# Performance work log

Hardware: AMD Instinct MI355X
Metric: run time of the kernel (lower is better)

Reference implementation:

```python
import jax, jax.numpy as jnp
import numpy as np

IMG = 1024.0          # image height == width
OUT = 7               # roi_size
RATIO = 2             # sampling_ratio
SCALE = 1.0 / 32.0    # spatial_scale
BBOX_W = (10.0, 10.0, 5.0, 5.0)
DWH_CLIP = float(np.log(1000.0 / 16.0))


def _bilinear(feat, ys, xs):
    """feat [C,H,W]; ys [N,P,1], xs [N,1,P] -> [C,N,P,P] (torchvision semantics)."""
    C, H, W = feat.shape
    valid = (ys > -1.0) & (ys < H) & (xs > -1.0) & (xs < W)
    y = jnp.clip(ys, 0.0, H - 1.0)
    x = jnp.clip(xs, 0.0, W - 1.0)
    y0 = jnp.floor(y).astype(jnp.int32)
    x0 = jnp.floor(x).astype(jnp.int32)
    y1 = jnp.minimum(y0 + 1, H - 1)
    x1 = jnp.minimum(x0 + 1, W - 1)
    ly = y - y0
    lx = x - x0
    hy = 1.0 - ly
    hx = 1.0 - lx
    v = (feat[:, y0, x0] * (hy * hx) + feat[:, y0, x1] * (hy * lx)
         + feat[:, y1, x0] * (ly * hx) + feat[:, y1, x1] * (ly * lx))
    return jnp.where(valid, v, 0.0)


def _roi_align_image(feat, rois):
    """feat [C,H,W], rois [N,4] xyxy in image coords -> [N,C,OUT,OUT]."""
    b = rois * SCALE
    x1, y1 = b[:, 0], b[:, 1]
    rw = jnp.maximum(b[:, 2] - x1, 1.0)
    rh = jnp.maximum(b[:, 3] - y1, 1.0)
    bw = rw / OUT
    bh = rh / OUT
    # sub-bin sample offsets: [OUT*RATIO] positions along each roi edge
    g = (jnp.arange(OUT, dtype=jnp.float32)[:, None]
         + (jnp.arange(RATIO, dtype=jnp.float32)[None, :] + 0.5) / RATIO).reshape(-1)
    ys = y1[:, None] + g[None, :] * bh[:, None]   # [N, OUT*RATIO]
    xs = x1[:, None] + g[None, :] * bw[:, None]
    v = _bilinear(feat, ys[:, :, None], xs[:, None, :])          # [C,N,P,P]
    C = feat.shape[0]
    v = v.reshape(C, -1, OUT, RATIO, OUT, RATIO).mean(axis=(3, 5))  # avg over samples
    return jnp.transpose(v, (1, 0, 2, 3))


def _decode(deltas, proposals):
    """deltas [R,K*4], proposals [R,4] -> clipped boxes [R,K,4]."""
    wx, wy, ww, wh = BBOX_W
    pw = proposals[:, 2] - proposals[:, 0]
    ph = proposals[:, 3] - proposals[:, 1]
    cx = proposals[:, 0] + 0.5 * pw
    cy = proposals[:, 1] + 0.5 * ph
    d = deltas.reshape(deltas.shape[0], -1, 4)
    dx = d[..., 0] / wx
    dy = d[..., 1] / wy
    dw = jnp.minimum(d[..., 2] / ww, DWH_CLIP)
    dh = jnp.minimum(d[..., 3] / wh, DWH_CLIP)
    pcx = dx * pw[:, None] + cx[:, None]
    pcy = dy * ph[:, None] + cy[:, None]
    ppw = jnp.exp(dw) * pw[:, None]
    pph = jnp.exp(dh) * ph[:, None]
    boxes = jnp.stack([pcx - 0.5 * ppw, pcy - 0.5 * pph,
                       pcx + 0.5 * ppw, pcy + 0.5 * pph], axis=-1)
    return jnp.clip(boxes, 0.0, IMG)  # clip_boxes_to_image


def setup_inputs() -> dict:
    key = jax.random.key(0)
    ks = jax.random.split(key, 8)
    B, N, C, H, W = 2, 1024, 256, 32, 32
    feat_dim = C * OUT * OUT  # 12544
    features = jax.random.normal(ks[0], (B, C, H, W), dtype=jnp.float32)
    cxy = jax.random.uniform(ks[1], (B, N, 2), minval=0.0, maxval=IMG)
    wh = jax.random.uniform(ks[2], (B, N, 2), minval=16.0, maxval=256.0)
    p1 = jnp.clip(cxy - 0.5 * wh, 0.0, IMG)
    p2 = jnp.clip(cxy + 0.5 * wh, 0.0, IMG)
    proposals = jnp.concatenate([p1, p2], axis=-1)  # [B,N,4] valid xyxy
    w1 = jax.random.normal(ks[3], (1024, feat_dim), dtype=jnp.float32) * 0.01
    w2 = jax.random.normal(ks[4], (1024, 1024), dtype=jnp.float32) * 0.01
    wc = jax.random.normal(ks[5], (2, 1024), dtype=jnp.float32) * 0.01
    wb = jax.random.normal(ks[6], (8, 1024), dtype=jnp.float32) * 0.001
    return {"features": features, "proposals": proposals,
            "w1": w1, "b1": jnp.zeros((1024,), jnp.float32),
            "w2": w2, "b2": jnp.zeros((1024,), jnp.float32),
            "wc": wc, "bc": jnp.zeros((2,), jnp.float32),
            "wb": wb, "bb": jnp.zeros((8,), jnp.float32)}


def reference(features, proposals, w1, b1, w2, b2, wc, bc, wb, bb):
    pooled = jax.vmap(_roi_align_image)(features, proposals)   # [B,N,C,7,7]
    B, N = pooled.shape[:2]
    x = pooled.reshape(B * N, -1)                               # flatten(start_dim=1)
    x = jax.nn.relu(x @ w1.T + b1)
    x = jax.nn.relu(x @ w2.T + b2)
    cls_scores = x @ wc.T + bc                                  # [R, num_classes]
    bbox_deltas = x @ wb.T + bb                                 # [R, num_classes*4]
    pred_boxes = _decode(bbox_deltas, proposals.reshape(-1, 4)) # [R, num_classes, 4]
    pred_scores = jax.nn.softmax(cls_scores, axis=-1)
    return cls_scores, bbox_deltas, pred_boxes, pred_scores
```

## Files before the change

kernel.cpp:

```cpp
#include <hip/hip_runtime.h>
#include <hip/hip_bf16.h>
#include <stdint.h>

typedef __attribute__((ext_vector_type(8))) short bf16x8;
typedef __attribute__((ext_vector_type(4))) float f32x4;

__device__ __forceinline__ ushort f2bf(float f) {
    union { float f; uint32_t u; } c; c.f = f;
    uint32_t u = c.u;
    uint32_t r = (u + 0x7FFFu + ((u >> 16) & 1u)) >> 16;
    return (ushort)r;
}

__device__ __forceinline__ void load16_to_lds(const void* gsrc, void* ldst) {
    __builtin_amdgcn_global_load_lds(
        (const __attribute__((address_space(1))) uint32_t*)gsrc,
        (__attribute__((address_space(3))) uint32_t*)ldst,
        16, 0, 0);
}

#define FENCE() asm volatile("" ::: "memory")
#define BARRIER() do { FENCE(); __builtin_amdgcn_s_barrier(); FENCE(); } while (0)
#define VMCNT(n) asm volatile("s_waitcnt vmcnt(" #n ")" ::: "memory")

__global__ __launch_bounds__(256) void f32_to_bf16_kernel(
    const float* __restrict__ in, ushort* __restrict__ out, int n)
{
    int i = (blockIdx.x * 256 + threadIdx.x) * 4;
    if (i >= n) return;
    float4 v = *(const float4*)(in + i);
    ushort4 o;
    o.x = f2bf(v.x); o.y = f2bf(v.y); o.z = f2bf(v.z); o.w = f2bf(v.w);
    *(ushort4*)(out + i) = o;
}

__global__ __launch_bounds__(256) void transpose_feat_kernel(
    const float* __restrict__ feat, float* __restrict__ featT)
{
    int bc = blockIdx.x;
    int b = bc >> 8;
    int c = bc & 255;
    const float* src = feat + (size_t)bc * 1024;
    float* dst = featT + (size_t)b * 262144 + c;
    #pragma unroll
    for (int i = 0; i < 4; ++i) {
        int p = i * 256 + threadIdx.x;
        dst[(size_t)p * 256] = src[p];
    }
}

__global__ __launch_bounds__(512) void roi_align_kernel(
    const float* __restrict__ featT, const float* __restrict__ props,
    ushort* __restrict__ pooled)
{
    int roi = blockIdx.x;
    int b = roi >> 10;
    __shared__ int   si0[28];
    __shared__ int   si1[28];
    __shared__ float sl[28];
    __shared__ float sv[28];
    __shared__ float Aw[7][10];
    __shared__ float Bw[7][10];
    __shared__ __align__(16) ushort outbuf[12544];
    int tid = threadIdx.x;
    if (tid < 28) {
        int axis = (tid >= 14) ? 1 : 0;
        int pp = tid - axis * 14;
        float c0 = props[roi * 4 + (axis ? 0 : 1)] * (1.f / 32.f);
        float c1 = props[roi * 4 + (axis ? 2 : 3)] * (1.f / 32.f);
        float sz = fmaxf(c1 - c0, 1.f);
        float bsz = sz * (1.f / 7.f);
        float g = (float)(pp >> 1) + ((float)(pp & 1) + 0.5f) * 0.5f;
        float c = c0 + g * bsz;
        float valid = (c > -1.f && c < 32.f) ? 1.f : 0.f;
        float cc = fminf(fmaxf(c, 0.f), 31.f);
        float fl = floorf(cc);
        int i0 = (int)fl;
        si0[tid] = i0;
        si1[tid] = min(i0 + 1, 31);
        sl[tid] = cc - fl;
        sv[tid] = valid;
    }
    __syncthreads();

    const int r0 = si0[0];
    const int c0 = si0[14];

    if (tid < 140) {
        int axis = tid / 70;
        int e = tid - axis * 70;
        int oy = e / 10, yy = e - oy * 10;
        int base = axis * 14;
        int org = axis ? c0 : r0;
        float wsum = 0.f;
        #pragma unroll
        for (int s = 0; s < 2; ++s) {
            int p = base + oy * 2 + s;
            float w = 0.f;
            if (si0[p] - org == yy) w += 1.f - sl[p];
            if (si1[p] - org == yy) w += sl[p];
            wsum += sv[p] * w;
        }
        wsum *= 0.5f;
        if (axis == 0) Aw[oy][yy] = wsum;
        else           Bw[oy][yy] = wsum;
    }
    __syncthreads();

    const int grp = tid >> 8;
    const int ch = tid & 255;
    const float* fbase = featT + (size_t)b * 262144 + ch;

    int xoff[10];
    #pragma unroll
    for (int x = 0; x < 10; ++x) xoff[x] = min(c0 + x, 31) * 256;

    if (grp == 0) {
        float t[4][10];
        #pragma unroll
        for (int oy = 0; oy < 4; ++oy)
            #pragma unroll
            for (int x = 0; x < 10; ++x) t[oy][x] = 0.f;
        #pragma unroll
        for (int y = 0; y < 10; ++y) {
            const float* frow = fbase + (size_t)min(r0 + y, 31) * 8192;
            float a0 = Aw[0][y], a1 = Aw[1][y], a2 = Aw[2][y], a3 = Aw[3][y];
            #pragma unroll
            for (int x = 0; x < 10; ++x) {
                float fv = frow[xoff[x]];
                t[0][x] += a0 * fv;
                t[1][x] += a1 * fv;
                t[2][x] += a2 * fv;
                t[3][x] += a3 * fv;
            }
        }
        #pragma unroll
        for (int oy = 0; oy < 4; ++oy)
            #pragma unroll
            for (int ox = 0; ox < 7; ++ox) {
                float o = 0.f;
                #pragma unroll
                for (int x = 0; x < 10; ++x) o += Bw[ox][x] * t[oy][x];
                outbuf[ch * 49 + oy * 7 + ox] = f2bf(o);
            }
    } else {
        float t[3][10];
        #pragma unroll
        for (int oy = 0; oy < 3; ++oy)
            #pragma unroll
            for (int x = 0; x < 10; ++x) t[oy][x] = 0.f;
        #pragma unroll
        for (int y = 0; y < 10; ++y) {
            const float* frow = fbase + (size_t)min(r0 + y, 31) * 8192;
            float a4 = Aw[4][y], a5 = Aw[5][y], a6 = Aw[6][y];
            #pragma unroll
            for (int x = 0; x < 10; ++x) {
                float fv = frow[xoff[x]];
                t[0][x] += a4 * fv;
                t[1][x] += a5 * fv;
                t[2][x] += a6 * fv;
            }
        }
        #pragma unroll
        for (int oy = 0; oy < 3; ++oy)
            #pragma unroll
            for (int ox = 0; ox < 7; ++ox) {
                float o = 0.f;
                #pragma unroll
                for (int x = 0; x < 10; ++x) o += Bw[ox][x] * t[oy][x];
                outbuf[ch * 49 + (4 + oy) * 7 + ox] = f2bf(o);
            }
    }
    __syncthreads();

    const uint4* src = (const uint4*)outbuf;
    uint4* dst = (uint4*)(pooled + (size_t)roi * 12544);
    #pragma unroll
    for (int i = 0; i < 4; ++i) {
        int idx = i * 512 + tid;
        if (idx < 1568) dst[idx] = src[idx];
    }
}

#define STAGE_A8(BB, HALF, KOFF) do { \
    _Pragma("unroll") for (int r_ = 0; r_ < 2; ++r_) { \
        int rbase_ = (HALF) * 128 + r_ * 64 + w * 8; \
        int row_ = rbase_ + (l >> 3); \
        int c16s_ = (l & 7) ^ (row_ & 7); \
        load16_to_lds((const char*)(Ap + (size_t)(m0 + row_) * K + (KOFF)) + c16s_ * 16, \
                      &sA[BB][rbase_][0]); \
    } } while (0)
#define STAGE_B8(BB, Q, KOFF) do { \
    _Pragma("unroll") for (int r_ = 0; r_ < 2; ++r_) { \
        int rl_ = r_ * 64 + w * 8 + (l >> 3); \
        int brow_ = ((rl_ >> 5) << 6) + (Q) * 32 + (rl_ & 31); \
        int c16s_ = (l & 7) ^ (rl_ & 7); \
        load16_to_lds((const char*)(Bp + (size_t)(n0 + brow_) * K + (KOFF)) + c16s_ * 16, \
                      &sB[BB][(Q) * 128 + r_ * 64 + w * 8][0]); \
    } } while (0)
#define PHASE8(QM, QN, STAGE_CODE, WAIT_CODE) do { \
    STAGE_CODE; \
    WAIT_CODE; \
    BARRIER(); \
    bf16x8 av_[8], bv_[4]; \
    _Pragma("unroll") for (int mm_ = 0; mm_ < 4; ++mm_) \
        _Pragma("unroll") for (int kk_ = 0; kk_ < 2; ++kk_) { \
            int lr_ = wm * 128 + (QM) * 64 + mm_ * 16 + lrow; \
            int c16s_ = (kk_ * 4 + khi) ^ (lrow & 7); \
            av_[mm_ * 2 + kk_] = *(const bf16x8*)&sA[cur][lr_][c16s_ * 8]; \
        } \
    _Pragma("unroll") for (int nn_ = 0; nn_ < 2; ++nn_) \
        _Pragma("unroll") for (int kk_ = 0; kk_ < 2; ++kk_) { \
            int lrB_ = (QN) * 128 + wn * 32 + nn_ * 16 + lrow; \
            int c16s_ = (kk_ * 4 + khi) ^ (lrow & 7); \
            bv_[nn_ * 2 + kk_] = *(const bf16x8*)&sB[cur][lrB_][c16s_ * 8]; \
        } \
    __builtin_amdgcn_s_setprio(1); \
    _Pragma("unroll") for (int mm_ = 0; mm_ < 4; ++mm_) \
        _Pragma("unroll") for (int nn_ = 0; nn_ < 2; ++nn_) \
            _Pragma("unroll") for (int kk_ = 0; kk_ < 2; ++kk_) \
                acc[(QM) * 4 + mm_][(QN) * 2 + nn_] = __builtin_amdgcn_mfma_f32_16x16x32_bf16( \
                    av_[mm_ * 2 + kk_], bv_[nn_ * 2 + kk_], acc[(QM) * 4 + mm_][(QN) * 2 + nn_], 0, 0, 0); \
    __builtin_amdgcn_s_setprio(0); \
    BARRIER(); \
} while (0)

__global__ __launch_bounds__(512) void gemm_8ph(
    const ushort* __restrict__ Ap, const ushort* __restrict__ Bp,
    float* __restrict__ part, int M, int N, int K, int klen)
{
    __shared__ __align__(16) ushort sA[2][256][64];
    __shared__ __align__(16) ushort sB[2][256][64];
    const int tid = threadIdx.x;

    const int nbx = gridDim.x, nby = gridDim.y;
    const int nwg = nbx * nby * gridDim.z;
    const int d = blockIdx.x + nbx * (blockIdx.y + nby * blockIdx.z);
    const int t = (d & 7) * (nwg >> 3) + (d >> 3);
    const int n_blk = t % nbx;
    const int m_blk = (t / nbx) % nby;
    const int k_blk = t / (nbx * nby);

    const int m0 = m_blk * 256;
    const int n0 = n_blk * 256;
    const int k_start = k_blk * klen;
    const int nt = klen >> 6;

    const int w = tid >> 6, l = tid & 63;
    const int wm = w >> 2, wn = w & 3;
    const int lrow = l & 15, khi = l >> 4;

    f32x4 acc[8][4] = {};

    {
        int k0 = k_start, k1 = k_start + 64;
        STAGE_B8(0, 0, k0);
        STAGE_A8(0, 1, k0);
        STAGE_A8(0, 0, k0);
        STAGE_B8(0, 1, k0);
        STAGE_B8(1, 0, k1);
        STAGE_A8(1, 1, k1);
    }

    int cur = 0;
    for (int T = 0; T < nt - 1; ++T) {
        const int koff1 = k_start + (T + 1) * 64;
        const int koff2 = k_start + (T + 2) * 64;
        const int nxt = cur ^ 1;
        const bool has2 = (T + 2) < nt;
        PHASE8(0, 0, { STAGE_A8(nxt, 0, koff1); }, VMCNT(8));
        PHASE8(1, 0, { STAGE_B8(nxt, 1, koff1); }, );
        PHASE8(1, 1, { if (has2) STAGE_B8(cur, 0, koff2); }, VMCNT(8));
        PHASE8(0, 1, { if (has2) STAGE_A8(cur, 1, koff2); }, );
        cur ^= 1;
    }
    PHASE8(0, 0, , VMCNT(2));
    PHASE8(1, 0, , );
    PHASE8(1, 1, , VMCNT(0));
    PHASE8(0, 1, , );

    const int r4 = (l >> 4) * 4;
    const int cc = l & 15;
    float* pb = part + (size_t)k_blk * M * N;
    #pragma unroll
    for (int m = 0; m < 8; ++m) {
        #pragma unroll
        for (int n = 0; n < 4; ++n) {
            int col = n0 + wn * 64 + n * 16 + cc;
            #pragma unroll
            for (int j = 0; j < 4; ++j) {
                int row = m0 + wm * 128 + m * 16 + r4 + j;
                pb[(size_t)row * N + col] = acc[m][n][j];
            }
        }
    }
}

__global__ __launch_bounds__(256) void gemm_bt_split(
    const ushort* __restrict__ A, const ushort* __restrict__ Bm,
    float* __restrict__ part, int M, int N, int K, int klen)
{
    constexpr int BK = 32;
    __shared__ __align__(16) ushort lA[2][128][BK];
    __shared__ __align__(16) ushort lB[2][128][BK];
    const int tid = threadIdx.x;

    const int nbx = gridDim.x, nby = gridDim.y;
    const int nwg = nbx * nby * gridDim.z;
    const int d = blockIdx.x + nbx * (blockIdx.y + nby * blockIdx.z);
    const int t = (d & 7) * (nwg >> 3) + (d >> 3);
    const int n_blk = t % nbx;
    const int m_blk = (t / nbx) % nby;
    const int k_blk = t / (nbx * nby);

    const int m0 = m_blk * 128;
    const int n0 = n_blk * 128;
    const int k_start = k_blk * klen;

    const int w = tid >> 6, l = tid & 63;
    const int wr = w >> 1, wcid = w & 1;
    const int lrow = l & 15;
    const int lkb = (((l >> 4) ^ ((lrow >> 1) & 3)) * 16);

    const int sc0 = tid, sc1 = 256 + tid;
    const int srow0 = sc0 >> 2, srow1 = sc1 >> 2;
    const int scol0 = ((sc0 & 3) ^ ((srow0 >> 1) & 3)) * 16;
    const int scol1 = ((sc1 & 3) ^ ((srow1 >> 1) & 3)) * 16;

    const int nsteps = klen / BK;

    {
        int k0 = k_start;
        load16_to_lds((const char*)(A + (size_t)(m0 + srow0) * K + k0) + scol0, ((char*)lA[0]) + sc0 * 16);
        load16_to_lds((const char*)(A + (size_t)(m0 + srow1) * K + k0) + scol1, ((char*)lA[0]) + sc1 * 16);
        load16_to_lds((const char*)(Bm + (size_t)(n0 + srow0) * K + k0) + scol0, ((char*)lB[0]) + sc0 * 16);
        load16_to_lds((const char*)(Bm + (size_t)(n0 + srow1) * K + k0) + scol1, ((char*)lB[0]) + sc1 * 16);
    }
    __syncthreads();

    f32x4 acc[4][4] = {};
    int cur = 0;

    for (int ts = 0; ts < nsteps; ++ts) {
        if (ts + 1 < nsteps) {
            int k0 = k_start + (ts + 1) * BK;
            int nxt = cur ^ 1;
            load16_to_lds((const char*)(A + (size_t)(m0 + srow0) * K + k0) + scol0, ((char*)lA[nxt]) + sc0 * 16);
            load16_to_lds((const char*)(A + (size_t)(m0 + srow1) * K + k0) + scol1, ((char*)lA[nxt]) + sc1 * 16);
            load16_to_lds((const char*)(Bm + (size_t)(n0 + srow0) * K + k0) + scol0, ((char*)lB[nxt]) + sc0 * 16);
            load16_to_lds((const char*)(Bm + (size_t)(n0 + srow1) * K + k0) + scol1, ((char*)lB[nxt]) + sc1 * 16);
        }

        bf16x8 af[4], bfr[4];
        #pragma unroll
        for (int m = 0; m < 4; ++m)
            af[m] = *(const bf16x8*)(((const char*)lA[cur]) + (wr * 64 + m * 16 + lrow) * 64 + lkb);
        #pragma unroll
        for (int n = 0; n < 4; ++n)
            bfr[n] = *(const bf16x8*)(((const char*)lB[cur]) + (wcid * 64 + n * 16 + lrow) * 64 + lkb);
        #pragma unroll
        for (int m = 0; m < 4; ++m)
            #pragma unroll
            for (int n = 0; n < 4; ++n)
                acc[m][n] = __builtin_amdgcn_mfma_f32_16x16x32_bf16(af[m], bfr[n], acc[m][n], 0, 0, 0);

        __syncthreads();
        cur ^= 1;
    }

    const int r4 = (l >> 4) * 4;
    const int cc = l & 15;
    float* pb = part + (size_t)k_blk * M * N;
    #pragma unroll
    for (int m = 0; m < 4; ++m) {
        #pragma unroll
        for (int n = 0; n < 4; ++n) {
            int col = n0 + wcid * 64 + n * 16 + cc;
            #pragma unroll
            for (int j = 0; j < 4; ++j) {
                int row = m0 + wr * 64 + m * 16 + r4 + j;
                pb[(size_t)row * N + col] = acc[m][n][j];
            }
        }
    }
}

template<bool OUT_BF16>
__global__ __launch_bounds__(256) void reduce_split_kernel(
    const float* __restrict__ part, const float* __restrict__ bias,
    void* __restrict__ out, int MN, int N, int S, int relu)
{
    int i4 = (blockIdx.x * 256 + threadIdx.x) * 4;
    if (i4 >= MN) return;
    float4 a = *(const float4*)(part + i4);
    for (int s = 1; s < S; ++s) {
        float4 b = *(const float4*)(part + (size_t)s * MN + i4);
        a.x += b.x; a.y += b.y; a.z += b.z; a.w += b.w;
    }
    int bc = i4 & (N - 1);
    float4 bv = *(const float4*)(bias + bc);
    a.x += bv.x; a.y += bv.y; a.z += bv.z; a.w += bv.w;
    if (relu) {
        a.x = fmaxf(a.x, 0.f); a.y = fmaxf(a.y, 0.f);
        a.z = fmaxf(a.z, 0.f); a.w = fmaxf(a.w, 0.f);
    }
    if (OUT_BF16) {
        ushort4 o; o.x = f2bf(a.x); o.y = f2bf(a.y); o.z = f2bf(a.z); o.w = f2bf(a.w);
        *(ushort4*)((ushort*)out + i4) = o;
    } else {
        *(float4*)((float*)out + i4) = a;
    }
}

template<bool OUT_BF16>
__global__ __launch_bounds__(256) void gemm_bt(
    const ushort* __restrict__ A, const ushort* __restrict__ Bm,
    const float* __restrict__ bias, void* __restrict__ Cout,
    int M, int N, int K, int relu)
{
    constexpr int BM = 128, BN = 64, BK = 32;
    __shared__ __align__(16) ushort lA[BM][BK];
    __shared__ __align__(16) ushort lB[BN][BK];
    const int tid = threadIdx.x;
    const int m0 = blockIdx.y * BM;
    const int n0 = blockIdx.x * BN;
    const int w = tid >> 6, l = tid & 63;
    const int wr = w >> 1, wcid = w & 1;
    const int lrow = l & 15, lk = (l >> 4) * 8;

    f32x4 acc[4][2] = {};

    for (int k0 = 0; k0 < K; k0 += BK) {
        __syncthreads();
        #pragma unroll
        for (int i = 0; i < 2; ++i) {
            int chunk = i * 256 + tid;
            int row = chunk >> 2;
            int colb = (chunk & 3) * 16;
            load16_to_lds((const char*)(A + (size_t)(m0 + row) * K + k0) + colb, ((char*)lA) + chunk * 16);
        }
        {
            int chunk = tid;
            int row = chunk >> 2;
            int colb = (chunk & 3) * 16;
            load16_to_lds((const char*)(Bm + (size_t)(n0 + row) * K + k0) + colb, ((char*)lB) + chunk * 16);
        }
        __syncthreads();

        bf16x8 af[4], bfr[2];
        #pragma unroll
        for (int m = 0; m < 4; ++m)
            af[m] = *(const bf16x8*)&lA[wr * 64 + m * 16 + lrow][lk];
        #pragma unroll
        for (int n = 0; n < 2; ++n)
            bfr[n] = *(const bf16x8*)&lB[wcid * 32 + n * 16 + lrow][lk];
        #pragma unroll
        for (int m = 0; m < 4; ++m)
            #pragma unroll
            for (int n = 0; n < 2; ++n)
                acc[m][n] = __builtin_amdgcn_mfma_f32_16x16x32_bf16(af[m], bfr[n], acc[m][n], 0, 0, 0);
    }

    const int r4 = (l >> 4) * 4;
    const int cc = l & 15;
    #pragma unroll
    for (int m = 0; m < 4; ++m) {
        #pragma unroll
        for (int n = 0; n < 2; ++n) {
            int col = n0 + wcid * 32 + n * 16 + cc;
            float bv = bias[col];
            #pragma unroll
            for (int j = 0; j < 4; ++j) {
                int row = m0 + wr * 64 + m * 16 + r4 + j;
                float v = acc[m][n][j] + bv;
                if (relu) v = fmaxf(v, 0.f);
                if (OUT_BF16) ((ushort*)Cout)[(size_t)row * N + col] = f2bf(v);
                else          ((float*)Cout)[(size_t)row * N + col] = v;
            }
        }
    }
}

__global__ __launch_bounds__(256) void heads_kernel(
    const float* __restrict__ x2,
    const float* __restrict__ wc, const float* __restrict__ bc,
    const float* __restrict__ wb, const float* __restrict__ bb,
    float* __restrict__ out)
{
    int w = threadIdx.x >> 6, l = threadIdx.x & 63;
    int row = blockIdx.x * 4 + w;
    const float* xr = x2 + (size_t)row * 1024;
    float acc[10];
    #pragma unroll
    for (int o = 0; o < 10; ++o) acc[o] = 0.f;
    for (int i = 0; i < 16; ++i) {
        int k = i * 64 + l;
        float xv = xr[k];
        #pragma unroll
        for (int o = 0; o < 2; ++o) acc[o] += xv * wc[o * 1024 + k];
        #pragma unroll
        for (int o = 0; o < 8; ++o) acc[2 + o] += xv * wb[o * 1024 + k];
    }
    #pragma unroll
    for (int o = 0; o < 10; ++o) {
        float v = acc[o];
        #pragma unroll
        for (int s = 32; s > 0; s >>= 1) v += __shfl_xor(v, s, 64);
        acc[o] = v;
    }
    if (l == 0) {
        float* cls = out;
        float* bbx = out + 2048 * 2;
        cls[row * 2 + 0] = acc[0] + bc[0];
        cls[row * 2 + 1] = acc[1] + bc[1];
        #pragma unroll
        for (int o = 0; o < 8; ++o) bbx[row * 8 + o] = acc[2 + o] + bb[o];
    }
}

__global__ __launch_bounds__(256) void decode_kernel(
    const float* __restrict__ props, float* __restrict__ out)
{
    int r = blockIdx.x * 256 + threadIdx.x;
    if (r >= 2048) return;
    const float* cls = out;
    const float* bbx = out + 4096;
    float* boxes  = out + 20480;
    float* scores = out + 36864;
    float px1 = props[r * 4 + 0], py1 = props[r * 4 + 1];
    float px2 = props[r * 4 + 2], py2 = props[r * 4 + 3];
    float pw = px2 - px1, ph = py2 - py1;
    float cx = px1 + 0.5f * pw, cy = py1 + 0.5f * ph;
    const float CLIP = 4.135166556742356f;
    #pragma unroll
    for (int k = 0; k < 2; ++k) {
        float dx = bbx[r * 8 + k * 4 + 0] * 0.1f;
        float dy = bbx[r * 8 + k * 4 + 1] * 0.1f;
        float dw = fminf(bbx[r * 8 + k * 4 + 2] * 0.2f, CLIP);
        float dh = fminf(bbx[r * 8 + k * 4 + 3] * 0.2f, CLIP);
        float pcx = dx * pw + cx, pcy = dy * ph + cy;
        float ppw = expf(dw) * pw, pph = expf(dh) * ph;
        float v0 = pcx - 0.5f * ppw, v1 = pcy - 0.5f * pph;
        float v2 = pcx + 0.5f * ppw, v3 = pcy + 0.5f * pph;
        boxes[r * 8 + k * 4 + 0] = fminf(fmaxf(v0, 0.f), 1024.f);
        boxes[r * 8 + k * 4 + 1] = fminf(fmaxf(v1, 0.f), 1024.f);
        boxes[r * 8 + k * 4 + 2] = fminf(fmaxf(v2, 0.f), 1024.f);
        boxes[r * 8 + k * 4 + 3] = fminf(fmaxf(v3, 0.f), 1024.f);
    }
    float s0 = cls[r * 2], s1 = cls[r * 2 + 1];
    float m = fmaxf(s0, s1);
    float e0 = expf(s0 - m), e1 = expf(s1 - m);
    float inv = 1.f / (e0 + e1);
    scores[r * 2 + 0] = e0 * inv;
    scores[r * 2 + 1] = e1 * inv;
}

extern "C" void kernel_launch(void* const* d_in, const int* in_sizes, int n_in,
                              void* d_out, int out_size, void* d_ws, size_t ws_size,
                              hipStream_t stream) {
    const float* feat  = (const float*)d_in[0];
    const float* props = (const float*)d_in[1];
    const float* w1    = (const float*)d_in[2];
    const float* b1    = (const float*)d_in[3];
    const float* w2    = (const float*)d_in[4];
    const float* b2    = (const float*)d_in[5];
    const float* wc    = (const float*)d_in[6];
    const float* bc    = (const float*)d_in[7];
    const float* wb    = (const float*)d_in[8];
    const float* bb    = (const float*)d_in[9];
    float* out = (float*)d_out;

    char* ws = (char*)d_ws;
    ushort* pooled = (ushort*)(ws);
    ushort* w1b    = (ushort*)(ws + 51380224);
    ushort* w2b    = (ushort*)(ws + 51380224 + 25690112);
    ushort* x1     = (ushort*)(ws + 79167488);
    float*  x2     = (float*) (ws + 83361792);
    float*  featT  = (float*) (ws + 83361792);
    float*  part   = (float*) (ws + 91750400);
    const size_t WS_NEED7 = 91750400 + (size_t)7 * 8388608;
    const size_t WS_NEED4 = 91750400 + 33554432;

    const int M = 2048, N = 1024;
    const int MN = M * N;

    f32_to_bf16_kernel<<<12845056 / 1024, 256, 0, stream>>>(w1, w1b, 12845056);
    f32_to_bf16_kernel<<<1048576 / 1024, 256, 0, stream>>>(w2, w2b, 1048576);
    transpose_feat_kernel<<<512, 256, 0, stream>>>(feat, featT);
    roi_align_kernel<<<2048, 512, 0, stream>>>(featT, props, pooled);

    if (ws_size >= WS_NEED7) {
        gemm_8ph<<<dim3(N / 256, M / 256, 7), 512, 0, stream>>>(pooled, w1b, part, M, N, 12544, 1792);
        reduce_split_kernel<true ><<<MN / 1024, 256, 0, stream>>>(part, b1, x1, MN, N, 7, 1);
        gemm_bt_split<<<dim3(N / 128, M / 128, 4), 256, 0, stream>>>(x1, w2b, part, M, N, 1024, 256);
        reduce_split_kernel<false><<<MN / 1024, 256, 0, stream>>>(part, b2, x2, MN, N, 4, 1);
    } else if (ws_size >= WS_NEED4) {
        gemm_bt_split<<<dim3(N / 128, M / 128, 4), 256, 0, stream>>>(pooled, w1b, part, M, N, 12544, 3136);
        reduce_split_kernel<true ><<<MN / 1024, 256, 0, stream>>>(part, b1, x1, MN, N, 4, 1);
        gemm_bt_split<<<dim3(N / 128, M / 128, 4), 256, 0, stream>>>(x1, w2b, part, M, N, 1024, 256);
        reduce_split_kernel<false><<<MN / 1024, 256, 0, stream>>>(part, b2, x2, MN, N, 4, 1);
    } else {
        gemm_bt<true ><<<dim3(N / 64, M / 128), 256, 0, stream>>>(pooled, w1b, b1, x1, M, N, 12544, 1);
        gemm_bt<false><<<dim3(N / 64, M / 128), 256, 0, stream>>>(x1, w2b, b2, x2, M, N, 1024, 1);
    }

    heads_kernel<<<512, 256, 0, stream>>>(x2, wc, bc, wb, bb, out);
    decode_kernel<<<8, 256, 0, stream>>>(props, out);
}
```

Baseline: 193.2 us.

## Restructure GEMM main loop to prefetch LDS fragments ahead and cut barriers

```diff
diff --git a/kernel.cpp b/kernel.cpp
--- a/kernel.cpp
+++ b/kernel.cpp
@@ -198,31 +198,28 @@
         load16_to_lds((const char*)(Bp + (size_t)(n0 + brow_) * K + (KOFF)) + c16s_ * 16, \
                       &sB[BB][(Q) * 128 + r_ * 64 + w * 8][0]); \
     } } while (0)
-#define PHASE8(QM, QN, STAGE_CODE, WAIT_CODE) do { \
-    STAGE_CODE; \
-    WAIT_CODE; \
-    BARRIER(); \
-    bf16x8 av_[8], bv_[4]; \
+#define LOADREGS(RA, RB, QM, QN) do { \
     _Pragma("unroll") for (int mm_ = 0; mm_ < 4; ++mm_) \
         _Pragma("unroll") for (int kk_ = 0; kk_ < 2; ++kk_) { \
             int lr_ = wm * 128 + (QM) * 64 + mm_ * 16 + lrow; \
-            int c16s_ = (kk_ * 4 + khi) ^ (lrow & 7); \
-            av_[mm_ * 2 + kk_] = *(const bf16x8*)&sA[cur][lr_][c16s_ * 8]; \
+            int c16_ = (kk_ * 4 + khi) ^ (lrow & 7); \
+            RA[mm_ * 2 + kk_] = *(const bf16x8*)&sA[cur][lr_][c16_ * 8]; \
         } \
     _Pragma("unroll") for (int nn_ = 0; nn_ < 2; ++nn_) \
         _Pragma("unroll") for (int kk_ = 0; kk_ < 2; ++kk_) { \
             int lrB_ = (QN) * 128 + wn * 32 + nn_ * 16 + lrow; \
-            int c16s_ = (kk_ * 4 + khi) ^ (lrow & 7); \
-            bv_[nn_ * 2 + kk_] = *(const bf16x8*)&sB[cur][lrB_][c16s_ * 8]; \
+            int c16_ = (kk_ * 4 + khi) ^ (lrow & 7); \
+            RB[nn_ * 2 + kk_] = *(const bf16x8*)&sB[cur][lrB_][c16_ * 8]; \
         } \
+} while (0)
+#define MFMAQ(RA, RB, QM, QN) do { \
     __builtin_amdgcn_s_setprio(1); \
     _Pragma("unroll") for (int mm_ = 0; mm_ < 4; ++mm_) \
         _Pragma("unroll") for (int nn_ = 0; nn_ < 2; ++nn_) \
             _Pragma("unroll") for (int kk_ = 0; kk_ < 2; ++kk_) \
                 acc[(QM) * 4 + mm_][(QN) * 2 + nn_] = __builtin_amdgcn_mfma_f32_16x16x32_bf16( \
-                    av_[mm_ * 2 + kk_], bv_[nn_ * 2 + kk_], acc[(QM) * 4 + mm_][(QN) * 2 + nn_], 0, 0, 0); \
+                    RA[mm_ * 2 + kk_], RB[nn_ * 2 + kk_], acc[(QM) * 4 + mm_][(QN) * 2 + nn_], 0, 0, 0); \
     __builtin_amdgcn_s_setprio(0); \
-    BARRIER(); \
 } while (0)
 
 __global__ __launch_bounds__(512) void gemm_8ph(
@@ -268,16 +265,41 @@
         const int koff2 = k_start + (T + 2) * 64;
         const int nxt = cur ^ 1;
         const bool has2 = (T + 2) < nt;
-        PHASE8(0, 0, { STAGE_A8(nxt, 0, koff1); }, VMCNT(8));
-        PHASE8(1, 0, { STAGE_B8(nxt, 1, koff1); }, );
-        PHASE8(1, 1, { if (has2) STAGE_B8(cur, 0, koff2); }, VMCNT(8));
-        PHASE8(0, 1, { if (has2) STAGE_A8(cur, 1, koff2); }, );
+        bf16x8 r0a[8], r0b[4], r1a[8], r1b[4], r2a[8], r2b[4], r3a[8], r3b[4];
+
+        STAGE_A8(nxt, 0, koff1);
+        VMCNT(8);
+        BARRIER();
+        LOADREGS(r0a, r0b, 0, 0);
+        LOADREGS(r1a, r1b, 1, 0);
+        MFMAQ(r0a, r0b, 0, 0);
+
+        STAGE_B8(nxt, 1, koff1);
+        VMCNT(8);
+        BARRIER();
+        LOADREGS(r2a, r2b, 1, 1);
+        MFMAQ(r1a, r1b, 1, 0);
+        BARRIER();
+
+        if (has2) STAGE_B8(cur, 0, koff2);
+        LOADREGS(r3a, r3b, 0, 1);
+        MFMAQ(r2a, r2b, 1, 1);
+        BARRIER();
+
+        if (has2) STAGE_A8(cur, 1, koff2);
+        MFMAQ(r3a, r3b, 0, 1);
+        BARRIER();
         cur ^= 1;
     }
-    PHASE8(0, 0, , VMCNT(2));
-    PHASE8(1, 0, , );
-    PHASE8(1, 1, , VMCNT(0));
-    PHASE8(0, 1, , );
+    VMCNT(0);
+    BARRIER();
+    {
+        bf16x8 ra[8], rb[4];
+        LOADREGS(ra, rb, 0, 0); MFMAQ(ra, rb, 0, 0);
+        LOADREGS(ra, rb, 1, 0); MFMAQ(ra, rb, 1, 0);
+        LOADREGS(ra, rb, 1, 1); MFMAQ(ra, rb, 1, 1);
+        LOADREGS(ra, rb, 0, 1); MFMAQ(ra, rb, 0, 1);
+    }
 
     const int r4 = (l >> 4) * 4;
     const int cc = l & 15;
```

Result: slower. 212.4 us (+10.0%).
